# Performance work log

Measured on AMD Instinct MI355X. Metric: run time of the kernel, lower is better.

## Reference

```python
import jax, jax.numpy as jnp
import numpy as np

NUM_CLASSES = 81
SCORE_THRESH = 0.05
BBOX_XFORM_CLIP = float(np.log(1000.0 / 16.0))
WX, WY, WW, WH = 10.0, 10.0, 5.0, 5.0           # post-processor box_coder weights


def setup_inputs() -> dict:
    key = jax.random.key(0)
    ks = jax.random.split(key, 10)
    R, C, P, H = 2000, 256, 7, 1024
    D = C * P * P  # 12544
    x = jax.random.normal(ks[0], (R, C, P, P), jnp.float32)
    xy = jax.random.uniform(ks[1], (R, 2), jnp.float32) * 600.0
    wh = jax.random.uniform(ks[2], (R, 2), jnp.float32) * 200.0 + 1.0
    boxes = jnp.concatenate([xy, xy + wh], axis=1)  # valid xyxy proposals
    s = 0.01
    W6 = jax.random.normal(ks[3], (D, H), jnp.float32) * s
    b6 = jnp.zeros((H,), jnp.float32)
    W7 = jax.random.normal(ks[4], (H, H), jnp.float32) * s
    b7 = jnp.zeros((H,), jnp.float32)
    Wcls = jax.random.normal(ks[5], (H, NUM_CLASSES), jnp.float32) * s
    bcls = jnp.zeros((NUM_CLASSES,), jnp.float32)
    Wbox = jax.random.normal(ks[6], (H, NUM_CLASSES * 4), jnp.float32) * s
    bbox_b = jnp.zeros((NUM_CLASSES * 4,), jnp.float32)
    return {"x": x, "boxes": boxes, "W6": W6, "b6": b6, "W7": W7, "b7": b7,
            "Wcls": Wcls, "bcls": bcls, "Wbox": Wbox, "bbox_b": bbox_b}


def _decode(reg, boxes):
    w = boxes[:, 2] - boxes[:, 0] + 1.0
    h = boxes[:, 3] - boxes[:, 1] + 1.0
    cx = boxes[:, 0] + 0.5 * w
    cy = boxes[:, 1] + 0.5 * h
    dx = reg[..., 0] / WX
    dy = reg[..., 1] / WY
    dw = jnp.minimum(reg[..., 2] / WW, BBOX_XFORM_CLIP)
    dh = jnp.minimum(reg[..., 3] / WH, BBOX_XFORM_CLIP)
    pcx = dx * w[:, None] + cx[:, None]
    pcy = dy * h[:, None] + cy[:, None]
    pw = jnp.exp(dw) * w[:, None]
    ph = jnp.exp(dh) * h[:, None]
    return jnp.stack([pcx - 0.5 * pw, pcy - 0.5 * ph,
                      pcx + 0.5 * pw - 1.0, pcy + 0.5 * ph - 1.0], axis=-1)


def reference(x, boxes, W6, b6, W7, b7, Wcls, bcls, Wbox, bbox_b):
    R = x.shape[0]
    f = x.reshape(R, -1)                          # [R, 12544]
    f6 = jax.nn.relu(f @ W6 + b6)                 # roi_output, [R, 1024]
    f7 = jax.nn.relu(f6 @ W7 + b7)                # [R, 1024]
    probs = jax.nn.softmax(f7 @ Wcls + bcls, axis=-1)       # [R, 81]
    reg = (f7 @ Wbox + bbox_b).reshape(R, NUM_CLASSES, 4)   # [R, 81, 4]
    dec = _decode(reg, boxes)                     # [R, 81, 4]
    # per_class_extend, fixed-shape: drop background class 0, mask below threshold
    pj = probs[:, 1:]                             # [R, 80]
    bj = dec[:, 1:, :]                            # [R, 80, 4]
    keep = pj > SCORE_THRESH
    scores_m = jnp.where(keep, pj, 0.0)
    boxes_m = jnp.where(keep[..., None], bj, 0.0).reshape(R, -1)  # [R, 320]
    return jnp.concatenate([scores_m, boxes_m, f6], axis=-1)      # [R, 1424]
```

## Files before the change

kernel.cpp:

```cpp
#include <hip/hip_runtime.h>
#include <stdint.h>

typedef float f32x4 __attribute__((ext_vector_type(4)));
typedef __bf16 bf16x8 __attribute__((ext_vector_type(8)));
typedef unsigned short us4 __attribute__((ext_vector_type(4)));

__device__ __forceinline__ unsigned short f32_to_bf16(float f) {
  union { float f; uint32_t u; } v; v.f = f;
  return (unsigned short)((v.u + 0x7FFFu + ((v.u >> 16) & 1u)) >> 16);
}

__device__ __forceinline__ void gload16(const void* g, void* l) {
  __builtin_amdgcn_global_load_lds((const __attribute__((address_space(1))) void*)g,
                                   (__attribute__((address_space(3))) void*)l, 16, 0, 0);
}

template <int EPI>
__global__ __launch_bounds__(256, 2) void gemm_bf16(
    const unsigned short* __restrict__ A, const unsigned short* __restrict__ Bt,
    int M, int NB, int K, int Mtiles, int Ntiles, int splits,
    float* __restrict__ outF, unsigned short* __restrict__ outH,
    const float* __restrict__ bias, const float* __restrict__ bias2,
    int NV, size_t splitStride)
{
  __shared__ unsigned short lds[16384];
  const int tid = threadIdx.x;
  const int lane = tid & 63;
  const int wave = tid >> 6;

  const int nwg = Mtiles * Ntiles * splits;
  const int per = nwg >> 3;
  int wg = (blockIdx.x & 7) * per + (blockIdx.x >> 3);
  const int nt = wg % Ntiles; wg /= Ntiles;
  const int mt = wg % Mtiles; wg /= Mtiles;
  const int sp = wg;

  const int nK = K >> 5;
  const int chunk = nK / splits;
  const int kBegin = sp * chunk;
  const int kEnd = kBegin + chunk;

  const int rowl = tid & 127;
  const int k8l = tid >> 7;
  int aRow = mt * 128 + rowl; if (aRow > M - 1) aRow = M - 1;
  int bRow = nt * 128 + rowl; if (bRow > NB - 1) bRow = NB - 1;
  const unsigned short* gA = A + (size_t)aRow * K + k8l * 8;
  const unsigned short* gB = Bt + (size_t)bRow * K + k8l * 8;

  const int k8 = lane >> 4;
  const int rsel = lane & 15;
  const int wrBase = (wave >> 1) * 64;
  const int wcBase = (wave & 1) * 64;
  int aOff[4], bOff[4];
#pragma unroll
  for (int m = 0; m < 4; ++m) aOff[m] = (k8 * 128 + wrBase + m * 16 + rsel) * 8;
#pragma unroll
  for (int n = 0; n < 4; ++n) bOff[n] = 4096 + (k8 * 128 + wcBase + n * 16 + rsel) * 8;

  f32x4 acc[4][4];
  const f32x4 zero = {0.f, 0.f, 0.f, 0.f};
#pragma unroll
  for (int m = 0; m < 4; ++m)
#pragma unroll
    for (int n = 0; n < 4; ++n) acc[m][n] = zero;

  auto stage = [&](int kt, int b) {
    const unsigned short* a = gA + kt * 32;
    const unsigned short* bsrc = gB + kt * 32;
    unsigned short* base = &lds[b * 8192];
    gload16(a,         base + tid * 8);
    gload16(a + 16,    base + (tid + 256) * 8);
    gload16(bsrc,      base + 4096 + tid * 8);
    gload16(bsrc + 16, base + 4096 + (tid + 256) * 8);
  };

  stage(kBegin, 0);
  __syncthreads();
  int cur = 0;
  for (int kt = kBegin; kt < kEnd; ++kt) {
    if (kt + 1 < kEnd) stage(kt + 1, cur ^ 1);
    const int cbase = cur * 8192;
    bf16x8 af[4], bfv[4];
#pragma unroll
    for (int m = 0; m < 4; ++m) af[m] = *(const bf16x8*)&lds[cbase + aOff[m]];
#pragma unroll
    for (int n = 0; n < 4; ++n) bfv[n] = *(const bf16x8*)&lds[cbase + bOff[n]];
#pragma unroll
    for (int m = 0; m < 4; ++m)
#pragma unroll
      for (int n = 0; n < 4; ++n)
        acc[m][n] = __builtin_amdgcn_mfma_f32_16x16x32_bf16(af[m], bfv[n], acc[m][n], 0, 0, 0);
    __syncthreads();
    cur ^= 1;
  }

  const int colBase = nt * 128 + wcBase + rsel;
  const int rowBase = mt * 128 + wrBase + (lane >> 4) * 4;
#pragma unroll
  for (int m = 0; m < 4; ++m) {
#pragma unroll
    for (int n = 0; n < 4; ++n) {
      const int col = colBase + n * 16;
#pragma unroll
      for (int j = 0; j < 4; ++j) {
        const int row = rowBase + m * 16 + j;
        if (row < M) {
          float v = acc[m][n][j];
          if (EPI == 0) {
            outF[sp * splitStride + (size_t)row * 1024 + col] = v;
          } else if (EPI == 1) {
            v += bias[col];
            v = fmaxf(v, 0.f);
            outH[(size_t)row * 1024 + col] = f32_to_bf16(v);
          } else {
            if (col < NV) {
              v += (col < 81) ? bias[col] : bias2[col - 81];
              outF[(size_t)row * NV + col] = v;
            }
          }
        }
      }
    }
  }
}

__global__ void transpose_to_bf16(const float* __restrict__ src, unsigned short* __restrict__ dst,
                                  int R, int C, int dstRowOff, int dstLd) {
  __shared__ unsigned short tile[64][66];
  const int c0 = blockIdx.x * 64, r0 = blockIdx.y * 64;
  const int t = threadIdx.x;
  const bool fast = ((C & 3) == 0) && (c0 + 64 <= C);
  const int lr0 = t >> 4;
  const int lc4 = (t & 15) * 4;
#pragma unroll
  for (int i = 0; i < 4; ++i) {
    const int lr = lr0 + i * 16;
    const size_t rowOff = (size_t)(r0 + lr) * C;
    if (fast) {
      f32x4 v = *(const f32x4*)(src + rowOff + c0 + lc4);
#pragma unroll
      for (int j = 0; j < 4; ++j) tile[lr][lc4 + j] = f32_to_bf16(v[j]);
    } else {
#pragma unroll
      for (int j = 0; j < 4; ++j) {
        const int c = c0 + lc4 + j;
        tile[lr][lc4 + j] = (c < C) ? f32_to_bf16(src[rowOff + c]) : (unsigned short)0;
      }
    }
  }
  __syncthreads();
  const int kk = (t & 15) * 4;
#pragma unroll
  for (int i = 0; i < 4; ++i) {
    const int lc = lr0 + i * 16;
    const int c = c0 + lc;
    if (c < C) {
      us4 h;
#pragma unroll
      for (int j = 0; j < 4; ++j) h[j] = tile[kk + j][lc];
      *(us4*)(dst + (size_t)(dstRowOff + c) * dstLd + r0 + kk) = h;
    }
  }
}

__global__ void convert_to_bf16(const float* __restrict__ src, unsigned short* __restrict__ dst,
                                long n4) {
  for (long i = blockIdx.x * (long)blockDim.x + threadIdx.x; i < n4;
       i += (long)gridDim.x * blockDim.x) {
    f32x4 v = *(const f32x4*)(src + i * 4);
    us4 h;
#pragma unroll
    for (int j = 0; j < 4; ++j) h[j] = f32_to_bf16(v[j]);
    *(us4*)(dst + i * 4) = h;
  }
}

__global__ void reduce_bias_act(const float* __restrict__ Cp, int splits, size_t sstride,
                                const float* __restrict__ bias, float* __restrict__ outF32,
                                unsigned short* __restrict__ outBf, int M) {
  const long total = (long)M * 256;
  for (long i = blockIdx.x * (long)blockDim.x + threadIdx.x; i < total;
       i += (long)gridDim.x * blockDim.x) {
    const long row = i >> 8;
    const int c4 = (int)(i & 255) * 4;
    const size_t off = ((size_t)row << 10) + c4;
    f32x4 s = *(const f32x4*)(Cp + off);
    for (int sp = 1; sp < splits; ++sp) s += *(const f32x4*)(Cp + (size_t)sp * sstride + off);
    s += *(const f32x4*)(bias + c4);
    us4 h;
#pragma unroll
    for (int j = 0; j < 4; ++j) { s[j] = fmaxf(s[j], 0.f); h[j] = f32_to_bf16(s[j]); }
    if (outF32) *(f32x4*)(outF32 + (size_t)row * 1424 + 400 + c4) = s;
    *(us4*)(outBf + off) = h;
  }
}

__global__ void head_epilogue(const float* __restrict__ cb, const float* __restrict__ boxes,
                              float* __restrict__ out, int M) {
  const float CLIP = 4.135166556742356f;
  const int row = blockIdx.x * 4 + (threadIdx.x >> 6);
  const int lane = threadIdx.x & 63;
  if (row >= M) return;
  const float* L = cb + (size_t)row * 405;
  const float v0 = L[lane];
  const float v1 = (lane < 17) ? L[64 + lane] : -1e30f;
  float mx = fmaxf(v0, v1);
#pragma unroll
  for (int off = 32; off; off >>= 1) mx = fmaxf(mx, __shfl_xor(mx, off, 64));
  float e0 = __expf(v0 - mx);
  float e1 = (lane < 17) ? __expf(v1 - mx) : 0.f;
  float sum = e0 + e1;
#pragma unroll
  for (int off = 32; off; off >>= 1) sum += __shfl_xor(sum, off, 64);
  const float inv = 1.f / sum;

  const float bx0 = boxes[row * 4 + 0], by0 = boxes[row * 4 + 1];
  const float bx1 = boxes[row * 4 + 2], by1 = boxes[row * 4 + 3];
  const float w = bx1 - bx0 + 1.f, h = by1 - by0 + 1.f;
  const float cx = bx0 + 0.5f * w, cy = by0 + 0.5f * h;
  float* orow = out + (size_t)row * 1424;

#pragma unroll
  for (int t = 0; t < 2; ++t) {
    const int c = (t == 0) ? lane : 64 + lane;
    const bool valid = (t == 0) ? (lane >= 1) : (lane < 17);
    if (valid) {
      const float p = ((t == 0) ? e0 : e1) * inv;
      const float* rg = L + 81 + c * 4;
      const float dx = rg[0] * 0.1f, dy = rg[1] * 0.1f;
      const float dw = fminf(rg[2] * 0.2f, CLIP), dh = fminf(rg[3] * 0.2f, CLIP);
      const float pcx = dx * w + cx, pcy = dy * h + cy;
      const float pw = __expf(dw) * w, ph = __expf(dh) * h;
      const bool keep = p > 0.05f;
      orow[c - 1] = keep ? p : 0.f;
      float* ob = orow + 80 + (c - 1) * 4;
      ob[0] = keep ? (pcx - 0.5f * pw) : 0.f;
      ob[1] = keep ? (pcy - 0.5f * ph) : 0.f;
      ob[2] = keep ? (pcx + 0.5f * pw - 1.f) : 0.f;
      ob[3] = keep ? (pcy + 0.5f * ph - 1.f) : 0.f;
    }
  }
}

extern "C" void kernel_launch(void* const* d_in, const int* in_sizes, int n_in,
                              void* d_out, int out_size, void* d_ws, size_t ws_size,
                              hipStream_t stream) {
  const float* x     = (const float*)d_in[0];
  const float* boxes = (const float*)d_in[1];
  const float* W6    = (const float*)d_in[2];
  const float* b6    = (const float*)d_in[3];
  const float* W7    = (const float*)d_in[4];
  const float* b7    = (const float*)d_in[5];
  const float* Wcls  = (const float*)d_in[6];
  const float* bcls  = (const float*)d_in[7];
  const float* Wbox  = (const float*)d_in[8];
  const float* bboxb = (const float*)d_in[9];
  float* out = (float*)d_out;

  const int M = 2000, D = 12544, H = 1024;
  char* p = (char*)d_ws;
  auto carve = [&](size_t bytes) { char* r = p; p += (bytes + 255) & ~(size_t)255; return r; };
  unsigned short* xb   = (unsigned short*)carve((size_t)M * D * 2);
  unsigned short* W6T  = (unsigned short*)carve((size_t)H * D * 2);
  unsigned short* W7T  = (unsigned short*)carve((size_t)H * H * 2);
  unsigned short* WcbT = (unsigned short*)carve((size_t)405 * H * 2);
  unsigned short* f6b  = (unsigned short*)carve((size_t)M * H * 2);
  unsigned short* f7b  = (unsigned short*)carve((size_t)M * H * 2);
  float* cbv           = (float*)carve((size_t)M * 405 * 4);
  size_t used = (size_t)(p - (char*)d_ws);
  int splits = 8;
  while (splits > 1 && used + (size_t)splits * M * H * 4 + 1024 > ws_size) splits >>= 1;
  float* Cp = (float*)carve((size_t)splits * M * H * 4);

  convert_to_bf16<<<4096, 256, 0, stream>>>(x, xb, (long)M * D / 4);
  transpose_to_bf16<<<dim3(16, 196), 256, 0, stream>>>(W6, W6T, D, H, 0, D);
  transpose_to_bf16<<<dim3(16, 16), 256, 0, stream>>>(W7, W7T, H, H, 0, H);
  transpose_to_bf16<<<dim3(2, 16), 256, 0, stream>>>(Wcls, WcbT, H, 81, 0, H);
  transpose_to_bf16<<<dim3(6, 16), 256, 0, stream>>>(Wbox, WcbT, H, 324, 81, H);

  gemm_bf16<0><<<16 * 8 * splits, 256, 0, stream>>>(xb, W6T, M, H, D, 16, 8, splits,
                                                    Cp, nullptr, nullptr, nullptr, 0,
                                                    (size_t)M * H);
  reduce_bias_act<<<2048, 256, 0, stream>>>(Cp, splits, (size_t)M * H, b6, out, f6b, M);

  const int splits2 = (splits >= 2) ? 2 : 1;
  if (splits2 == 2) {
    gemm_bf16<0><<<16 * 8 * 2, 256, 0, stream>>>(f6b, W7T, M, H, H, 16, 8, 2,
                                                 Cp, nullptr, nullptr, nullptr, 0,
                                                 (size_t)M * H);
    reduce_bias_act<<<2048, 256, 0, stream>>>(Cp, 2, (size_t)M * H, b7, nullptr, f7b, M);
  } else {
    gemm_bf16<1><<<16 * 8, 256, 0, stream>>>(f6b, W7T, M, H, H, 16, 8, 1,
                                             nullptr, f7b, b7, nullptr, 0, 0);
  }

  gemm_bf16<2><<<16 * 4, 256, 0, stream>>>(f7b, WcbT, M, 405, H, 16, 4, 1,
                                           cbv, nullptr, bcls, bboxb, 405, 0);

  head_epilogue<<<(M + 3) / 4, 256, 0, stream>>>(cbv, boxes, out, M);
}
```

Baseline: 407.3 us.

## Double GEMM K-tile to 64, merge prep kernels, cut split-K

```diff
diff --git a/kernel.cpp b/kernel.cpp
--- a/kernel.cpp
+++ b/kernel.cpp
@@ -23,7 +23,7 @@
     const float* __restrict__ bias, const float* __restrict__ bias2,
     int NV, size_t splitStride)
 {
-  __shared__ unsigned short lds[16384];
+  __shared__ unsigned short lds[32768];
   const int tid = threadIdx.x;
   const int lane = tid & 63;
   const int wave = tid >> 6;
@@ -35,7 +35,7 @@
   const int mt = wg % Mtiles; wg /= Mtiles;
   const int sp = wg;
 
-  const int nK = K >> 5;
+  const int nK = K >> 6;
   const int chunk = nK / splits;
   const int kBegin = sp * chunk;
   const int kEnd = kBegin + chunk;
@@ -47,15 +47,20 @@
   const unsigned short* gA = A + (size_t)aRow * K + k8l * 8;
   const unsigned short* gB = Bt + (size_t)bRow * K + k8l * 8;
 
-  const int k8 = lane >> 4;
+  const int k8f = lane >> 4;
   const int rsel = lane & 15;
   const int wrBase = (wave >> 1) * 64;
   const int wcBase = (wave & 1) * 64;
-  int aOff[4], bOff[4];
-#pragma unroll
-  for (int m = 0; m < 4; ++m) aOff[m] = (k8 * 128 + wrBase + m * 16 + rsel) * 8;
-#pragma unroll
-  for (int n = 0; n < 4; ++n) bOff[n] = 4096 + (k8 * 128 + wcBase + n * 16 + rsel) * 8;
+  int aOff[2][4], bOff[2][4];
+#pragma unroll
+  for (int kk = 0; kk < 2; ++kk) {
+#pragma unroll
+    for (int m = 0; m < 4; ++m)
+      aOff[kk][m] = ((kk * 4 + k8f) * 128 + wrBase + m * 16 + rsel) * 8;
+#pragma unroll
+    for (int n = 0; n < 4; ++n)
+      bOff[kk][n] = 8192 + ((kk * 4 + k8f) * 128 + wcBase + n * 16 + rsel) * 8;
+  }
 
   f32x4 acc[4][4];
   const f32x4 zero = {0.f, 0.f, 0.f, 0.f};
@@ -65,13 +70,14 @@
     for (int n = 0; n < 4; ++n) acc[m][n] = zero;
 
   auto stage = [&](int kt, int b) {
-    const unsigned short* a = gA + kt * 32;
-    const unsigned short* bsrc = gB + kt * 32;
-    unsigned short* base = &lds[b * 8192];
-    gload16(a,         base + tid * 8);
-    gload16(a + 16,    base + (tid + 256) * 8);
-    gload16(bsrc,      base + 4096 + tid * 8);
-    gload16(bsrc + 16, base + 4096 + (tid + 256) * 8);
+    const unsigned short* a = gA + (size_t)kt * 64;
+    const unsigned short* bsrc = gB + (size_t)kt * 64;
+    unsigned short* base = &lds[b * 16384];
+#pragma unroll
+    for (int j = 0; j < 4; ++j) {
+      gload16(a + j * 16,    base + (tid + j * 256) * 8);
+      gload16(bsrc + j * 16, base + 8192 + (tid + j * 256) * 8);
+    }
   };
 
   stage(kBegin, 0);
@@ -79,17 +85,20 @@
   int cur = 0;
   for (int kt = kBegin; kt < kEnd; ++kt) {
     if (kt + 1 < kEnd) stage(kt + 1, cur ^ 1);
-    const int cbase = cur * 8192;
-    bf16x8 af[4], bfv[4];
-#pragma unroll
-    for (int m = 0; m < 4; ++m) af[m] = *(const bf16x8*)&lds[cbase + aOff[m]];
-#pragma unroll
-    for (int n = 0; n < 4; ++n) bfv[n] = *(const bf16x8*)&lds[cbase + bOff[n]];
-#pragma unroll
-    for (int m = 0; m < 4; ++m)
-#pragma unroll
-      for (int n = 0; n < 4; ++n)
-        acc[m][n] = __builtin_amdgcn_mfma_f32_16x16x32_bf16(af[m], bfv[n], acc[m][n], 0, 0, 0);
+    const int cb = cur * 16384;
+#pragma unroll
+    for (int kk = 0; kk < 2; ++kk) {
+      bf16x8 af[4], bfv[4];
+#pragma unroll
+      for (int m = 0; m < 4; ++m) af[m] = *(const bf16x8*)&lds[cb + aOff[kk][m]];
+#pragma unroll
+      for (int n = 0; n < 4; ++n) bfv[n] = *(const bf16x8*)&lds[cb + bOff[kk][n]];
+#pragma unroll
+      for (int m = 0; m < 4; ++m)
+#pragma unroll
+        for (int n = 0; n < 4; ++n)
+          acc[m][n] = __builtin_amdgcn_mfma_f32_16x16x32_bf16(af[m], bfv[n], acc[m][n], 0, 0, 0);
+    }
     __syncthreads();
     cur ^= 1;
   }
@@ -124,10 +133,11 @@
   }
 }
 
-__global__ void transpose_to_bf16(const float* __restrict__ src, unsigned short* __restrict__ dst,
-                                  int R, int C, int dstRowOff, int dstLd) {
-  __shared__ unsigned short tile[64][66];
-  const int c0 = blockIdx.x * 64, r0 = blockIdx.y * 64;
+__device__ __forceinline__ void transpose_tile(
+    const float* __restrict__ src, unsigned short* __restrict__ dst,
+    int R, int C, int dstRowOff, int dstLd, int bx, int by,
+    unsigned short (*tile)[66]) {
+  const int c0 = bx * 64, r0 = by * 64;
   const int t = threadIdx.x;
   const bool fast = ((C & 3) == 0) && (c0 + 64 <= C);
   const int lr0 = t >> 4;
@@ -163,15 +173,34 @@
   }
 }
 
-__global__ void convert_to_bf16(const float* __restrict__ src, unsigned short* __restrict__ dst,
-                                long n4) {
-  for (long i = blockIdx.x * (long)blockDim.x + threadIdx.x; i < n4;
-       i += (long)gridDim.x * blockDim.x) {
-    f32x4 v = *(const f32x4*)(src + i * 4);
-    us4 h;
-#pragma unroll
-    for (int j = 0; j < 4; ++j) h[j] = f32_to_bf16(v[j]);
-    *(us4*)(dst + i * 4) = h;
+__global__ __launch_bounds__(256) void prep(
+    const float* __restrict__ x, unsigned short* __restrict__ xb, long n4,
+    const float* __restrict__ W6, unsigned short* __restrict__ W6T,
+    const float* __restrict__ W7, unsigned short* __restrict__ W7T,
+    const float* __restrict__ Wcls, const float* __restrict__ Wbox,
+    unsigned short* __restrict__ WcbT) {
+  __shared__ unsigned short tile[64][66];
+  const int b = blockIdx.x;
+  if (b < 2048) {
+    for (long i = (long)b * 256 + threadIdx.x; i < n4; i += 2048L * 256) {
+      f32x4 v = *(const f32x4*)(x + i * 4);
+      us4 h;
+#pragma unroll
+      for (int j = 0; j < 4; ++j) h[j] = f32_to_bf16(v[j]);
+      *(us4*)(xb + i * 4) = h;
+    }
+  } else if (b < 2048 + 3136) {
+    const int i = b - 2048;
+    transpose_tile(W6, W6T, 12544, 1024, 0, 12544, i & 15, i >> 4, tile);
+  } else if (b < 2048 + 3136 + 256) {
+    const int i = b - (2048 + 3136);
+    transpose_tile(W7, W7T, 1024, 1024, 0, 1024, i & 15, i >> 4, tile);
+  } else if (b < 2048 + 3136 + 256 + 32) {
+    const int i = b - (2048 + 3136 + 256);
+    transpose_tile(Wcls, WcbT, 1024, 81, 0, 1024, i & 1, i >> 1, tile);
+  } else {
+    const int i = b - (2048 + 3136 + 256 + 32);
+    transpose_tile(Wbox, WcbT, 1024, 324, 81, 1024, i % 6, i / 6, tile);
   }
 }
 
@@ -268,31 +297,20 @@
   unsigned short* f7b  = (unsigned short*)carve((size_t)M * H * 2);
   float* cbv           = (float*)carve((size_t)M * 405 * 4);
   size_t used = (size_t)(p - (char*)d_ws);
-  int splits = 8;
+  int splits = 4;
   while (splits > 1 && used + (size_t)splits * M * H * 4 + 1024 > ws_size) splits >>= 1;
   float* Cp = (float*)carve((size_t)splits * M * H * 4);
 
-  convert_to_bf16<<<4096, 256, 0, stream>>>(x, xb, (long)M * D / 4);
-  transpose_to_bf16<<<dim3(16, 196), 256, 0, stream>>>(W6, W6T, D, H, 0, D);
-  transpose_to_bf16<<<dim3(16, 16), 256, 0, stream>>>(W7, W7T, H, H, 0, H);
-  transpose_to_bf16<<<dim3(2, 16), 256, 0, stream>>>(Wcls, WcbT, H, 81, 0, H);
-  transpose_to_bf16<<<dim3(6, 16), 256, 0, stream>>>(Wbox, WcbT, H, 324, 81, H);
+  prep<<<2048 + 3136 + 256 + 32 + 96, 256, 0, stream>>>(
+      x, xb, (long)M * D / 4, W6, W6T, W7, W7T, Wcls, Wbox, WcbT);
 
   gemm_bf16<0><<<16 * 8 * splits, 256, 0, stream>>>(xb, W6T, M, H, D, 16, 8, splits,
                                                     Cp, nullptr, nullptr, nullptr, 0,
                                                     (size_t)M * H);
   reduce_bias_act<<<2048, 256, 0, stream>>>(Cp, splits, (size_t)M * H, b6, out, f6b, M);
 
-  const int splits2 = (splits >= 2) ? 2 : 1;
-  if (splits2 == 2) {
-    gemm_bf16<0><<<16 * 8 * 2, 256, 0, stream>>>(f6b, W7T, M, H, H, 16, 8, 2,
-                                                 Cp, nullptr, nullptr, nullptr, 0,
-                                                 (size_t)M * H);
-    reduce_bias_act<<<2048, 256, 0, stream>>>(Cp, 2, (size_t)M * H, b7, nullptr, f7b, M);
-  } else {
-    gemm_bf16<1><<<16 * 8, 256, 0, stream>>>(f6b, W7T, M, H, H, 16, 8, 1,
-                                             nullptr, f7b, b7, nullptr, 0, 0);
-  }
+  gemm_bf16<1><<<16 * 8, 256, 0, stream>>>(f6b, W7T, M, H, H, 16, 8, 1,
+                                           nullptr, f7b, b7, nullptr, 0, 0);
 
   gemm_bf16<2><<<16 * 4, 256, 0, stream>>>(f7b, WcbT, M, 405, H, 16, 4, 1,
                                            cbv, nullptr, bcls, bboxb, 405, 0);
```

Result: no change. 405.4 us (-0.5%).
